# Optimization experiments

Hardware: AMD Instinct MI355X
Metric: run time of the kernel (lower is better)

The kernel has to match this reference:

```python
import math
import jax, jax.numpy as jnp
import numpy as np

H = 12          # num_attention_heads
D = 128         # head_dim = 1536 // 12
E = H * D       # hidden_size
CHUNK = 12      # attention_chunk_size
PAST = 12       # attention_context_left - 1
FUT = 0         # attention_context_right
CTX = CHUNK + PAST + FUT   # 24
CAP = 50.0      # attention_logit_cap
Q_SCALE = D ** (-0.5) / math.log(2.0)
K_SCALE = math.log(1.0 + math.e) / math.log(2.0)


def setup_inputs() -> dict:
    key = jax.random.key(0)
    ks = jax.random.split(key, 8)
    B, S = 8, 3072
    w_scale = E ** (-0.5)
    return {
        "hidden_states": jax.random.normal(ks[0], (B, S, E), jnp.float32),
        "position_embeddings": jax.random.normal(ks[1], (CTX, E), jnp.float32),
        "w_q": jax.random.normal(ks[2], (E, E), jnp.float32) * w_scale,
        "w_k": jax.random.normal(ks[3], (E, E), jnp.float32) * w_scale,
        "w_v": jax.random.normal(ks[4], (E, E), jnp.float32) * w_scale,
        "w_post": jax.random.normal(ks[5], (E, E), jnp.float32) * w_scale,
        "w_rel": jax.random.normal(ks[6], (E, E), jnp.float32) * w_scale,
        "per_dim_scale": jnp.zeros((D,), jnp.float32),
    }


def _rel_shift(x):
    # x: [B, H, nb, chunk, P] with P <= CTX+1 -> [B, H, nb, chunk, CTX]
    B, h, nb, bs, p = x.shape
    x = jnp.pad(x, ((0, 0), (0, 0), (0, 0), (0, 0), (0, CTX + 1 - p)))
    x = x.reshape(B, h, nb, bs * (CTX + 1))[..., : bs * CTX]
    return x.reshape(B, h, nb, bs, CTX)


def reference(hidden_states, position_embeddings, w_q, w_k, w_v, w_post, w_rel, per_dim_scale):
    B, S, _ = hidden_states.shape
    # projections (torch Linear: y = x @ W.T), computed in float32
    q = (hidden_states @ w_q.T).reshape(B, S, H, D)
    k = (hidden_states @ w_k.T).reshape(B, S, H, D)
    v = (hidden_states @ w_v.T).reshape(B, S, H, D)
    q = q * (Q_SCALE * jax.nn.softplus(per_dim_scale))  # per-dim query scale
    k = k * K_SCALE

    nb = (S + CHUNK - 1) // CHUNK
    pad = nb * CHUNK - S
    # convert_to_block: [B, nb, CHUNK, H, D]
    qb = jnp.pad(q, ((0, 0), (0, pad), (0, 0), (0, 0))).reshape(B, nb, CHUNK, H, D)

    def ctx_extract(x):
        # pad left by PAST, right by FUT + CHUNK - 1, then gather CTX-wide windows strided by CHUNK
        xp = jnp.pad(x, ((0, 0), (PAST, FUT + CHUNK - 1), (0, 0), (0, 0)))
        idx = jnp.arange(nb)[:, None] * CHUNK + jnp.arange(CTX)[None, :]
        return xp[:, idx]  # [B, nb, CTX, H, D]

    kc = ctx_extract(k)
    vc = ctx_extract(v)

    rel_k = (position_embeddings @ w_rel.T).reshape(-1, H, D)  # [P, H, D]

    # content term: [B, H, nb, CHUNK, CTX]
    ac = jnp.einsum('bnchd,bnkhd->bhnck', qb, kc)
    # position term + Transformer-XL rel shift
    bd = jnp.einsum('bnchd,phd->bhncp', qb, rel_k)
    bd = _rel_shift(bd)

    logits = ac + bd
    logits = jnp.tanh(logits / CAP) * CAP  # softcap
    attn_weights = jax.nn.softmax(logits, axis=-1)

    out = jnp.einsum('bhnck,bnkhd->bnchd', attn_weights, vc)
    out = out.reshape(B, nb * CHUNK, H * D)[:, :S]
    out = out @ w_post.T
    return out, attn_weights
```

## Files before the change

kernel.cpp:

```cpp
#include <hip/hip_runtime.h>
#include <hip/hip_bf16.h>

#define HH 12
#define DD 128
#define EE 1536
#define QKVP 4608
#define NBATCH 8
#define SEQ 3072
#define NBLK 256
#define CHK 12
#define CTXW 24
#define MTOK 24576

#define Q_SCALE_BASE 0.12751743f
#define K_SCALE_F 1.8946361322f

#define PITCH 65

typedef short s16x8 __attribute__((ext_vector_type(8)));
typedef float f32x4 __attribute__((ext_vector_type(4)));

__device__ __forceinline__ float bf2f(unsigned short u) {
  return __builtin_bit_cast(float, ((unsigned int)u) << 16);
}
__device__ __forceinline__ unsigned short f2bf(float f) {
  unsigned int u = __builtin_bit_cast(unsigned int, f);
  u += 0x7fffu + ((u >> 16) & 1u);
  return (unsigned short)(u >> 16);
}
__device__ __forceinline__ void bf2f2(unsigned int u, float& lo, float& hi) {
  lo = __builtin_bit_cast(float, u << 16);
  hi = __builtin_bit_cast(float, u & 0xffff0000u);
}

__device__ __forceinline__ void async16(const void* g, void* l) {
  __builtin_amdgcn_global_load_lds(
      (const __attribute__((address_space(1))) unsigned int*)g,
      (__attribute__((address_space(3))) unsigned int*)l, 16, 0, 0);
}

__global__ __launch_bounds__(256) void k_cvt(const float4* __restrict__ in,
                                             ushort4* __restrict__ out, int n4) {
  int i = blockIdx.x * 256 + threadIdx.x;
  if (i < n4) {
    float4 v = in[i];
    ushort4 o;
    o.x = f2bf(v.x); o.y = f2bf(v.y); o.z = f2bf(v.z); o.w = f2bf(v.w);
    out[i] = o;
  }
}

__global__ void k_qscale(const float* __restrict__ pds, float* __restrict__ qs) {
  int d = threadIdx.x;
  if (d < DD) {
    float x = pds[d];
    float sp = (x > 20.f) ? x : log1pf(expf(x));
    qs[d] = Q_SCALE_BASE * sp;
  }
}

__global__ __launch_bounds__(256) void k_rel(const float* __restrict__ pos,
                                             const float* __restrict__ w_rel,
                                             unsigned short* __restrict__ rel16) {
  __shared__ unsigned short lp[12 * EE];
  const int t = threadIdx.x;
  const int p0 = blockIdx.y * 12;
  for (int i = t; i < 12 * EE / 4; i += 256) {
    float4 x = ((const float4*)(pos + (long)p0 * EE))[i];
    ushort4 o; o.x = f2bf(x.x); o.y = f2bf(x.y); o.z = f2bf(x.z); o.w = f2bf(x.w);
    ((ushort4*)lp)[i] = o;
  }
  __syncthreads();
  const int col = blockIdx.x * 128 + (t & 127);
  const int pg = t >> 7;
  float acc[6] = {0.f, 0.f, 0.f, 0.f, 0.f, 0.f};
  const float* wr = w_rel + (long)col * EE;
  for (int e = 0; e < EE; ++e) {
    float w = wr[e];
#pragma unroll
    for (int i = 0; i < 6; ++i) acc[i] += w * bf2f(lp[(pg * 6 + i) * EE + e]);
  }
#pragma unroll
  for (int i = 0; i < 6; ++i)
    rel16[(long)(p0 + pg * 6 + i) * EE + col] = f2bf(acc[i]);
}


__device__ __forceinline__ void stage_half(const unsigned short* g0, long Kl,
                                           unsigned short* lhalf,
                                           int w, int rlo, int qz) {
  const unsigned short* s0 = g0 + (long)(w * 16 + rlo) * Kl + qz * 8;
  async16(s0,          lhalf + w * 1024);
  async16(s0 + 8 * Kl, lhalf + w * 1024 + 512);
}

__device__ __forceinline__ void tile4(
    unsigned short* AP, unsigned short* BP,
    unsigned short* AQ, unsigned short* BQ,
    const unsigned short* gAt, const unsigned short* gBt, long Kl,
    int t1, int t2, int w, int rlo, int qz,
    int aBase, int bBase, int sw0, int sw1, f32x4 (&acc)[8][4]) {
  s16x8 af[4], bf[4];

#pragma unroll
  for (int i = 0; i < 4; ++i) af[i] = *(const s16x8*)&AP[(aBase + 16 * i) * 64 + sw0];
#pragma unroll
  for (int j = 0; j < 4; ++j) bf[j] = *(const s16x8*)&BP[(bBase + 16 * j) * 64 + sw0];
  stage_half(gAt + (long)t1 * 64, Kl, AQ, w, rlo, qz);
  __builtin_amdgcn_s_barrier();
  __builtin_amdgcn_s_setprio(1);
#pragma unroll
  for (int i = 0; i < 4; ++i)
#pragma unroll
    for (int j = 0; j < 4; ++j)
      acc[i][j] = __builtin_amdgcn_mfma_f32_16x16x32_bf16(af[i], bf[j], acc[i][j], 0, 0, 0);
  __builtin_amdgcn_s_setprio(0);
  __builtin_amdgcn_s_barrier();

#pragma unroll
  for (int i = 0; i < 4; ++i) af[i] = *(const s16x8*)&AP[(aBase + 64 + 16 * i) * 64 + sw0];
  stage_half(gAt + 128 * Kl + (long)t1 * 64, Kl, AQ + 8192, w, rlo, qz);
  __builtin_amdgcn_s_barrier();
  __builtin_amdgcn_s_setprio(1);
#pragma unroll
  for (int i = 0; i < 4; ++i)
#pragma unroll
    for (int j = 0; j < 4; ++j)
      acc[4 + i][j] = __builtin_amdgcn_mfma_f32_16x16x32_bf16(af[i], bf[j], acc[4 + i][j], 0, 0, 0);
  __builtin_amdgcn_s_setprio(0);
  __builtin_amdgcn_s_barrier();

#pragma unroll
  for (int i = 0; i < 4; ++i) af[i] = *(const s16x8*)&AP[(aBase + 16 * i) * 64 + sw1];
#pragma unroll
  for (int j = 0; j < 4; ++j) bf[j] = *(const s16x8*)&BP[(bBase + 16 * j) * 64 + sw1];
  __builtin_amdgcn_s_barrier();
  __builtin_amdgcn_s_setprio(1);
#pragma unroll
  for (int i = 0; i < 4; ++i)
#pragma unroll
    for (int j = 0; j < 4; ++j)
      acc[i][j] = __builtin_amdgcn_mfma_f32_16x16x32_bf16(af[i], bf[j], acc[i][j], 0, 0, 0);
  __builtin_amdgcn_s_setprio(0);
  __builtin_amdgcn_s_barrier();

#pragma unroll
  for (int i = 0; i < 4; ++i) af[i] = *(const s16x8*)&AP[(aBase + 64 + 16 * i) * 64 + sw1];
  stage_half(gBt + (long)t2 * 64, Kl, BP, w, rlo, qz);
  stage_half(gBt + 128 * Kl + (long)t2 * 64, Kl, BP + 8192, w, rlo, qz);
  asm volatile("s_waitcnt vmcnt(4)" ::: "memory");
  __builtin_amdgcn_s_barrier();
  __builtin_amdgcn_s_setprio(1);
#pragma unroll
  for (int i = 0; i < 4; ++i)
#pragma unroll
    for (int j = 0; j < 4; ++j)
      acc[4 + i][j] = __builtin_amdgcn_mfma_f32_16x16x32_bf16(af[i], bf[j], acc[4 + i][j], 0, 0, 0);
  __builtin_amdgcn_s_setprio(0);
  __builtin_amdgcn_s_barrier();
}

__global__ __launch_bounds__(512, 2) void k_gemm256(
    const unsigned short* __restrict__ A, const unsigned short* __restrict__ Bt,
    void* __restrict__ Cv, int M, int N, int K, int gN,
    int mode, const float* __restrict__ qscale, int c_f32) {
  __shared__ unsigned short sm[65536];

  const int tid = threadIdx.x;
  const int w = tid >> 6;
  const int lane = tid & 63;
  const int quad = lane >> 4;
  const int l16 = lane & 15;
  const int sw = l16 & 7;
  const int rlo = lane >> 3;
  const int qz = (lane & 7) ^ rlo;

  const int nwg = gridDim.x;
  const int orig = blockIdx.x;
  const int qd = nwg >> 3;
  const int xcd = orig & 7;
  const int u = orig >> 3;
  const int bandsz = 4 * gN;
  const int band = u / bandsz;
  const int rem = u - band * bandsz;
  const int mi = band * 4 + (rem & 3);
  const int ni = rem >> 2;
  const int mloc = qd / gN;
  const int mt = xcd * mloc + mi;
  const int nt = ni;
  const long bm = (long)mt * 256, bn = (long)nt * 256;
  const long Kl = K;
  const unsigned short* gAt = A + bm * Kl;
  const unsigned short* gBt = Bt + bn * Kl;

  unsigned short* A0 = sm;
  unsigned short* B0 = sm + 16384;
  unsigned short* A1 = sm + 32768;
  unsigned short* B1 = sm + 49152;

  const int aBase = (w >> 2) * 128 + l16;
  const int bBase = (w & 3) * 64 + l16;
  const int sw0 = ((quad ^ sw) & 7) * 8;
  const int sw1 = (((4 | quad) ^ sw) & 7) * 8;

  f32x4 acc[8][4] = {};
  const int NT = K >> 6;

  stage_half(gAt,            Kl, A0,        w, rlo, qz);
  stage_half(gAt + 128 * Kl, Kl, A0 + 8192, w, rlo, qz);
  stage_half(gBt,            Kl, B0,        w, rlo, qz);
  stage_half(gBt + 128 * Kl, Kl, B0 + 8192, w, rlo, qz);
  stage_half(gBt + 64,            Kl, B1,        w, rlo, qz);
  stage_half(gBt + 128 * Kl + 64, Kl, B1 + 8192, w, rlo, qz);
  asm volatile("s_waitcnt vmcnt(4)" ::: "memory");
  __builtin_amdgcn_s_barrier();

  for (int t = 0; t < NT; t += 2) {
    const int t1 = t + 1;
    const int t2 = (t + 2 == NT) ? 0 : t + 2;
    const int t3 = (t + 3 >= NT) ? t + 3 - NT : t + 3;
    tile4(A0, B0, A1, B1, gAt, gBt, Kl, t1, t2, w, rlo, qz, aBase, bBase, sw0, sw1, acc);
    tile4(A1, B1, A0, B0, gAt, gBt, Kl, t2, t3, w, rlo, qz, aBase, bBase, sw0, sw1, acc);
  }

  __syncthreads();

  const int wmq = (w >> 2) * 128;
  const int wnq = (w & 3) * 64;

  if (!c_f32) {
#pragma unroll
    for (int j = 0; j < 4; ++j) {
      const long col = bn + wnq + 16 * j + l16;
      float scale = 1.0f;
      if (mode == 3)
        scale = (col < 1536) ? qscale[col & (DD - 1)] : (col < 3072 ? K_SCALE_F : 1.0f);
      const int lc = wnq + 16 * j + l16;
#pragma unroll
      for (int i = 0; i < 8; ++i) {
        const int lr0 = wmq + 16 * i + quad * 4;
#pragma unroll
        for (int r = 0; r < 4; ++r) {
          const int lr = lr0 + r;
          const int gsw = (lc >> 3) ^ ((lr >> 2) & 7);
          sm[lr * 256 + gsw * 8 + (lc & 7)] = f2bf(acc[i][j][r] * scale);
        }
      }
    }
    __syncthreads();
#pragma unroll
    for (int k = 0; k < 16; ++k) {
      const int G = k * 512 + tid;
      const int row = G >> 5, gc = G & 31;
      const int gsw = gc ^ ((row >> 2) & 7);
      s16x8 vdat = *(const s16x8*)&sm[row * 256 + gsw * 8];
      *(s16x8*)&((unsigned short*)Cv)[(bm + row) * (long)N + bn + gc * 8] = vdat;
    }
  } else {
    float* Cf = (float*)sm;
#pragma unroll
    for (int h = 0; h < 2; ++h) {
      if ((wmq == 0) == (h == 0)) {
#pragma unroll
        for (int j = 0; j < 4; ++j) {
          const long col = bn + wnq + 16 * j + l16;
          float scale = 1.0f;
          if (mode == 3)
            scale = (col < 1536) ? qscale[col & (DD - 1)] : (col < 3072 ? K_SCALE_F : 1.0f);
          const int lc = wnq + 16 * j + l16;
#pragma unroll
          for (int i = 0; i < 8; ++i) {
            const int lr0 = 16 * i + quad * 4;
#pragma unroll
            for (int r = 0; r < 4; ++r) {
              const int lr = lr0 + r;
              const int gsw = (lc >> 2) ^ ((lr >> 2) & 7);
              Cf[lr * 256 + gsw * 4 + (lc & 3)] = acc[i][j][r] * scale;
            }
          }
        }
      }
      __syncthreads();
#pragma unroll
      for (int k = 0; k < 16; ++k) {
        const int G = k * 512 + tid;
        const int row = G >> 6, gc = G & 63;
        const int gsw = gc ^ ((row >> 2) & 7);
        float4 vdat = *(const float4*)&Cf[row * 256 + gsw * 4];
        *(float4*)&((float*)Cv)[(bm + h * 128 + row) * (long)N + bn + gc * 4] = vdat;
      }
      __syncthreads();
    }
  }
}

__global__ __launch_bounds__(256) void k_attn(
    const unsigned short* __restrict__ qkv, const unsigned short* __restrict__ rel,
    unsigned short* __restrict__ attn_out, float* __restrict__ aw_out) {
  const int n = blockIdx.x;
  const int b = blockIdx.y;
  const int h = blockIdx.z;
  const int t = threadIdx.x;

  __shared__ unsigned int lq[CHK * PITCH];
  __shared__ unsigned int lk[CTXW * PITCH];
  __shared__ unsigned int lv[CTXW * PITCH];
  __shared__ unsigned int lr[CTXW * PITCH];
  __shared__ float sac[CHK * CTXW];
  __shared__ float sbd[CHK * CTXW];
  __shared__ float smax[CHK];
  __shared__ float sinv[CHK];

  const long tok0 = (long)b * SEQ + (long)n * CHK;
  const long hq = (long)h * DD;

  for (int u = t; u < CHK * 16; u += 256) {
    int r = u >> 4, w4 = u & 15;
    uint4 x = *(const uint4*)&qkv[(tok0 + r) * QKVP + hq + w4 * 8];
    unsigned int* d = &lq[r * PITCH + w4 * 4];
    d[0] = x.x; d[1] = x.y; d[2] = x.z; d[3] = x.w;
  }
  for (int u = t; u < CTXW * 16; u += 256) {
    int r = u >> 4, w4 = u & 15;
    int s = n * CHK + r - 12;
    uint4 kx, vx;
    if (s >= 0) {
      const unsigned short* base = &qkv[((long)b * SEQ + s) * QKVP + hq];
      kx = *(const uint4*)&base[1536 + w4 * 8];
      vx = *(const uint4*)&base[3072 + w4 * 8];
    } else {
      kx = make_uint4(0, 0, 0, 0);
      vx = make_uint4(0, 0, 0, 0);
    }
    uint4 rx = *(const uint4*)&rel[(long)r * EE + hq + w4 * 8];
    unsigned int* dk = &lk[r * PITCH + w4 * 4];
    unsigned int* dv = &lv[r * PITCH + w4 * 4];
    unsigned int* dr = &lr[r * PITCH + w4 * 4];
    dk[0] = kx.x; dk[1] = kx.y; dk[2] = kx.z; dk[3] = kx.w;
    dv[0] = vx.x; dv[1] = vx.y; dv[2] = vx.z; dv[3] = vx.w;
    dr[0] = rx.x; dr[1] = rx.y; dr[2] = rx.z; dr[3] = rx.w;
  }
  __syncthreads();

  for (int p = t; p < CHK * CTXW; p += 256) {
    int c = p / CTXW, j = p - c * CTXW;
    const unsigned int* uq = &lq[c * PITCH];
    const unsigned int* uk = &lk[j * PITCH];
    const unsigned int* ur = &lr[j * PITCH];
    float ac = 0.f, bd = 0.f;
#pragma unroll 16
    for (int d2 = 0; d2 < DD / 2; ++d2) {
      float a0, a1, k0f, k1f, r0, r1;
      bf2f2(uq[d2], a0, a1);
      bf2f2(uk[d2], k0f, k1f);
      bf2f2(ur[d2], r0, r1);
      ac += a0 * k0f + a1 * k1f;
      bd += a0 * r0 + a1 * r1;
    }
    sac[p] = ac;
    sbd[p] = bd;
  }
  __syncthreads();

  for (int p = t; p < CHK * CTXW; p += 256) {
    int c = p / CTXW, j = p - c * CTXW;
    float y;
    if (j >= c) y = sbd[c * CTXW + (j - c)];
    else if (j == c - 1) y = 0.f;
    else y = sbd[(c - 1) * CTXW + (j - c + CTXW + 1)];
    float x = (sac[p] + y) * 0.02f;
    x = fminf(fmaxf(x, -15.f), 15.f);
    float e2 = __expf(2.f * x);
    sac[p] = 50.f * (e2 - 1.f) / (e2 + 1.f);
  }
  __syncthreads();

  if (t < CHK) {
    float m = -3.0e38f;
#pragma unroll
    for (int j = 0; j < CTXW; ++j) m = fmaxf(m, sac[t * CTXW + j]);
    smax[t] = m;
  }
  __syncthreads();

  for (int p = t; p < CHK * CTXW; p += 256) {
    int c = p / CTXW;
    sbd[p] = __expf(sac[p] - smax[c]);
  }
  __syncthreads();

  if (t < CHK) {
    float s = 0.f;
#pragma unroll
    for (int j = 0; j < CTXW; ++j) s += sbd[t * CTXW + j];
    sinv[t] = 1.f / s;
  }
  __syncthreads();

  for (int p = t; p < CHK * CTXW; p += 256) {
    int c = p / CTXW, j = p - c * CTXW;
    float w = sbd[p] * sinv[c];
    sac[p] = w;
    aw_out[((((long)b * HH + h) * NBLK + n) * CHK + c) * CTXW + j] = w;
  }
  __syncthreads();

  for (int p = t; p < CHK * (DD / 2); p += 256) {
    int c = p >> 6, d2 = p & 63;
    float a0 = 0.f, a1 = 0.f;
#pragma unroll
    for (int j = 0; j < CTXW; ++j) {
      float w = sac[c * CTXW + j];
      float v0, v1;
      bf2f2(lv[j * PITCH + d2], v0, v1);
      a0 += w * v0; a1 += w * v1;
    }
    unsigned int packed = ((unsigned int)f2bf(a1) << 16) | (unsigned int)f2bf(a0);
    *(unsigned int*)&attn_out[(tok0 + c) * EE + hq + d2 * 2] = packed;
  }
}

extern "C" void kernel_launch(void* const* d_in, const int* in_sizes, int n_in,
                              void* d_out, int out_size, void* d_ws, size_t ws_size,
                              hipStream_t stream) {
  const float* hs     = (const float*)d_in[0];
  const float* pos    = (const float*)d_in[1];
  const float* w_q    = (const float*)d_in[2];
  const float* w_k    = (const float*)d_in[3];
  const float* w_v    = (const float*)d_in[4];
  const float* w_post = (const float*)d_in[5];
  const float* w_rel  = (const float*)d_in[6];
  const float* pds    = (const float*)d_in[7];

  char* ws = (char*)d_ws;
  const size_t TOKB = (size_t)MTOK * EE * 2;
  const size_t WB   = (size_t)EE * EE * 2;
  unsigned short* hs16   = (unsigned short*)(ws);
  unsigned short* qkv16  = (unsigned short*)(ws + TOKB);
  unsigned short* wq16   = (unsigned short*)(ws + 4 * TOKB);
  unsigned short* wk16   = (unsigned short*)(ws + 4 * TOKB + WB);
  unsigned short* wv16   = (unsigned short*)(ws + 4 * TOKB + 2 * WB);
  unsigned short* wp16   = (unsigned short*)(ws + 4 * TOKB + 3 * WB);
  unsigned short* rel16  = (unsigned short*)(ws + 4 * TOKB + 4 * WB);
  float* qscale          = (float*)(ws + 4 * TOKB + 4 * WB + CTXW * EE * 2);
  unsigned short* attn16 = hs16;

  float* out = (float*)d_out;
  float* aw  = out + (size_t)MTOK * EE;

  k_cvt<<<36864, 256, 0, stream>>>((const float4*)hs, (ushort4*)hs16, MTOK * EE / 4);
  k_cvt<<<2304, 256, 0, stream>>>((const float4*)w_q, (ushort4*)wq16, EE * EE / 4);
  k_cvt<<<2304, 256, 0, stream>>>((const float4*)w_k, (ushort4*)wk16, EE * EE / 4);
  k_cvt<<<2304, 256, 0, stream>>>((const float4*)w_v, (ushort4*)wv16, EE * EE / 4);
  k_cvt<<<2304, 256, 0, stream>>>((const float4*)w_post, (ushort4*)wp16, EE * EE / 4);
  k_qscale<<<1, 128, 0, stream>>>(pds, qscale);
  k_rel<<<dim3(12, 2), 256, 0, stream>>>(pos, w_rel, rel16);

  k_gemm256<<<dim3((MTOK / 256) * (QKVP / 256)), 512, 0, stream>>>(
      hs16, wq16, qkv16, MTOK, QKVP, EE, QKVP / 256, 3, qscale, 0);

  k_attn<<<dim3(NBLK, NBATCH, HH), 256, 0, stream>>>(qkv16, rel16, attn16, aw);

  k_gemm256<<<dim3((MTOK / 256) * (EE / 256)), 512, 0, stream>>>(
      attn16, wp16, out, MTOK, EE, EE, EE / 256, 0, nullptr, 1);
}
```

Before: 1.033 ms.

## Use MFMA for attention QK/PV and vectorize relative-position projection

Rewrites the chunked attention kernel so the content and position logits (Q·K and Q·rel) and the weights-times-V product run as bf16 16x16x32 MFMA instructions, replacing scalar per-thread dot products. Q, K and rel tiles are stored in XOR-swizzled LDS, and V is stored transposed so it can serve as an MFMA operand. The k_rel kernel also reads w_rel as float4 and LDS as packed pairs to cut per-element load overhead. The softmax weights are now rounded to bf16 before the PV product, which slightly lowers precision, and the padded tile rows are left uninitialized, though they only feed results that are discarded.

```diff
diff --git a/kernel.cpp b/kernel.cpp
--- a/kernel.cpp
+++ b/kernel.cpp
@@ -15,8 +15,6 @@
 #define Q_SCALE_BASE 0.12751743f
 #define K_SCALE_F 1.8946361322f
 
-#define PITCH 65
-
 typedef short s16x8 __attribute__((ext_vector_type(8)));
 typedef float f32x4 __attribute__((ext_vector_type(4)));
 
@@ -75,10 +73,17 @@
   const int pg = t >> 7;
   float acc[6] = {0.f, 0.f, 0.f, 0.f, 0.f, 0.f};
   const float* wr = w_rel + (long)col * EE;
-  for (int e = 0; e < EE; ++e) {
-    float w = wr[e];
-#pragma unroll
-    for (int i = 0; i < 6; ++i) acc[i] += w * bf2f(lp[(pg * 6 + i) * EE + e]);
+  for (int e = 0; e < EE; e += 4) {
+    float4 w4 = *(const float4*)&wr[e];
+#pragma unroll
+    for (int i = 0; i < 6; ++i) {
+      const unsigned short* lpr = &lp[(pg * 6 + i) * EE + e];
+      unsigned int u01 = *(const unsigned int*)lpr;
+      unsigned int u23 = *(const unsigned int*)(lpr + 2);
+      float a0, a1, a2, a3;
+      bf2f2(u01, a0, a1); bf2f2(u23, a2, a3);
+      acc[i] += w4.x * a0 + w4.y * a1 + w4.z * a2 + w4.w * a3;
+    }
   }
 #pragma unroll
   for (int i = 0; i < 6; ++i)
@@ -301,122 +306,139 @@
   const int b = blockIdx.y;
   const int h = blockIdx.z;
   const int t = threadIdx.x;
-
-  __shared__ unsigned int lq[CHK * PITCH];
-  __shared__ unsigned int lk[CTXW * PITCH];
-  __shared__ unsigned int lv[CTXW * PITCH];
-  __shared__ unsigned int lr[CTXW * PITCH];
-  __shared__ float sac[CHK * CTXW];
-  __shared__ float sbd[CHK * CTXW];
-  __shared__ float smax[CHK];
-  __shared__ float sinv[CHK];
+  const int wv = t >> 6;
+  const int lane = t & 63;
+  const int quad = lane >> 4;
+  const int l16 = lane & 15;
+
+  __shared__ unsigned short lq[16 * 128];
+  __shared__ unsigned short lk[32 * 128];
+  __shared__ unsigned short lrel[32 * 128];
+  __shared__ unsigned short lvt[128 * 40];
+  __shared__ unsigned short lw[16 * 40];
+  __shared__ float sac[16 * 33];
+  __shared__ float sbd[16 * 33];
+  __shared__ unsigned short sO[12 * 136];
+  __shared__ float smax[12], sinv[12];
 
   const long tok0 = (long)b * SEQ + (long)n * CHK;
   const long hq = (long)h * DD;
 
-  for (int u = t; u < CHK * 16; u += 256) {
+  for (int u = t; u < 192; u += 256) {
     int r = u >> 4, w4 = u & 15;
     uint4 x = *(const uint4*)&qkv[(tok0 + r) * QKVP + hq + w4 * 8];
-    unsigned int* d = &lq[r * PITCH + w4 * 4];
-    d[0] = x.x; d[1] = x.y; d[2] = x.z; d[3] = x.w;
-  }
-  for (int u = t; u < CTXW * 16; u += 256) {
+    *(uint4*)&lq[r * 128 + ((w4 ^ (r & 7)) * 8)] = x;
+  }
+  for (int u = t; u < 384; u += 256) {
     int r = u >> 4, w4 = u & 15;
     int s = n * CHK + r - 12;
-    uint4 kx, vx;
-    if (s >= 0) {
-      const unsigned short* base = &qkv[((long)b * SEQ + s) * QKVP + hq];
-      kx = *(const uint4*)&base[1536 + w4 * 8];
-      vx = *(const uint4*)&base[3072 + w4 * 8];
-    } else {
-      kx = make_uint4(0, 0, 0, 0);
-      vx = make_uint4(0, 0, 0, 0);
-    }
+    uint4 kx = make_uint4(0, 0, 0, 0);
+    if (s >= 0) kx = *(const uint4*)&qkv[((long)b * SEQ + s) * QKVP + hq + 1536 + w4 * 8];
+    *(uint4*)&lk[r * 128 + ((w4 ^ (r & 7)) * 8)] = kx;
     uint4 rx = *(const uint4*)&rel[(long)r * EE + hq + w4 * 8];
-    unsigned int* dk = &lk[r * PITCH + w4 * 4];
-    unsigned int* dv = &lv[r * PITCH + w4 * 4];
-    unsigned int* dr = &lr[r * PITCH + w4 * 4];
-    dk[0] = kx.x; dk[1] = kx.y; dk[2] = kx.z; dk[3] = kx.w;
-    dv[0] = vx.x; dv[1] = vx.y; dv[2] = vx.z; dv[3] = vx.w;
-    dr[0] = rx.x; dr[1] = rx.y; dr[2] = rx.z; dr[3] = rx.w;
-  }
-  __syncthreads();
-
-  for (int p = t; p < CHK * CTXW; p += 256) {
-    int c = p / CTXW, j = p - c * CTXW;
-    const unsigned int* uq = &lq[c * PITCH];
-    const unsigned int* uk = &lk[j * PITCH];
-    const unsigned int* ur = &lr[j * PITCH];
-    float ac = 0.f, bd = 0.f;
-#pragma unroll 16
-    for (int d2 = 0; d2 < DD / 2; ++d2) {
-      float a0, a1, k0f, k1f, r0, r1;
-      bf2f2(uq[d2], a0, a1);
-      bf2f2(uk[d2], k0f, k1f);
-      bf2f2(ur[d2], r0, r1);
-      ac += a0 * k0f + a1 * k1f;
-      bd += a0 * r0 + a1 * r1;
-    }
-    sac[p] = ac;
-    sbd[p] = bd;
+    *(uint4*)&lrel[r * 128 + ((w4 ^ (r & 7)) * 8)] = rx;
+  }
+  for (int u = t; u < 384; u += 256) {
+    int r = u >> 4, d16 = u & 15, d0 = d16 * 8;
+    int s = n * CHK + r - 12;
+    uint4 vx = make_uint4(0, 0, 0, 0);
+    if (s >= 0) vx = *(const uint4*)&qkv[((long)b * SEQ + s) * QKVP + hq + 3072 + d0];
+    unsigned short vs[8];
+    *(uint4*)vs = vx;
+#pragma unroll
+    for (int i = 0; i < 8; ++i) {
+      int ii = (i + d16) & 7;
+      lvt[(d0 + ii) * 40 + r] = vs[ii];
+    }
+  }
+  for (int u = t; u < 128; u += 256)
+    *(uint4*)&lvt[u * 40 + 24] = make_uint4(0, 0, 0, 0);
+  for (int u = t; u < 80; u += 256)
+    *(uint4*)&lw[u * 8] = make_uint4(0, 0, 0, 0);
+  __syncthreads();
+
+  {
+    const unsigned short* bsrc = (wv < 2) ? lk : lrel;
+    const int nt = wv & 1;
+    f32x4 acc = {};
+#pragma unroll
+    for (int dc = 0; dc < 4; ++dc) {
+      const int g = dc * 4 + quad;
+      s16x8 a = *(const s16x8*)&lq[l16 * 128 + ((g ^ (l16 & 7)) * 8)];
+      const int rB = nt * 16 + l16;
+      s16x8 bb = *(const s16x8*)&bsrc[rB * 128 + ((g ^ (rB & 7)) * 8)];
+      acc = __builtin_amdgcn_mfma_f32_16x16x32_bf16(a, bb, acc, 0, 0, 0);
+    }
+    float* dstp = (wv < 2) ? sac : sbd;
+#pragma unroll
+    for (int r = 0; r < 4; ++r)
+      dstp[(quad * 4 + r) * 33 + nt * 16 + l16] = acc[r];
   }
   __syncthreads();
 
   for (int p = t; p < CHK * CTXW; p += 256) {
     int c = p / CTXW, j = p - c * CTXW;
     float y;
-    if (j >= c) y = sbd[c * CTXW + (j - c)];
+    if (j >= c) y = sbd[c * 33 + (j - c)];
     else if (j == c - 1) y = 0.f;
-    else y = sbd[(c - 1) * CTXW + (j - c + CTXW + 1)];
-    float x = (sac[p] + y) * 0.02f;
+    else y = sbd[(c - 1) * 33 + (j - c + CTXW + 1)];
+    float x = (sac[c * 33 + j] + y) * 0.02f;
     x = fminf(fmaxf(x, -15.f), 15.f);
     float e2 = __expf(2.f * x);
-    sac[p] = 50.f * (e2 - 1.f) / (e2 + 1.f);
+    sac[c * 33 + j] = 50.f * (e2 - 1.f) / (e2 + 1.f);
   }
   __syncthreads();
 
   if (t < CHK) {
     float m = -3.0e38f;
 #pragma unroll
-    for (int j = 0; j < CTXW; ++j) m = fmaxf(m, sac[t * CTXW + j]);
+    for (int j = 0; j < CTXW; ++j) m = fmaxf(m, sac[t * 33 + j]);
     smax[t] = m;
   }
   __syncthreads();
 
   for (int p = t; p < CHK * CTXW; p += 256) {
-    int c = p / CTXW;
-    sbd[p] = __expf(sac[p] - smax[c]);
+    int c = p / CTXW, j = p - c * CTXW;
+    sbd[c * 33 + j] = __expf(sac[c * 33 + j] - smax[c]);
   }
   __syncthreads();
 
   if (t < CHK) {
     float s = 0.f;
 #pragma unroll
-    for (int j = 0; j < CTXW; ++j) s += sbd[t * CTXW + j];
+    for (int j = 0; j < CTXW; ++j) s += sbd[t * 33 + j];
     sinv[t] = 1.f / s;
   }
   __syncthreads();
 
   for (int p = t; p < CHK * CTXW; p += 256) {
     int c = p / CTXW, j = p - c * CTXW;
-    float w = sbd[p] * sinv[c];
-    sac[p] = w;
-    aw_out[((((long)b * HH + h) * NBLK + n) * CHK + c) * CTXW + j] = w;
-  }
-  __syncthreads();
-
-  for (int p = t; p < CHK * (DD / 2); p += 256) {
-    int c = p >> 6, d2 = p & 63;
-    float a0 = 0.f, a1 = 0.f;
-#pragma unroll
-    for (int j = 0; j < CTXW; ++j) {
-      float w = sac[c * CTXW + j];
-      float v0, v1;
-      bf2f2(lv[j * PITCH + d2], v0, v1);
-      a0 += w * v0; a1 += w * v1;
-    }
-    unsigned int packed = ((unsigned int)f2bf(a1) << 16) | (unsigned int)f2bf(a0);
-    *(unsigned int*)&attn_out[(tok0 + c) * EE + hq + d2 * 2] = packed;
+    float wgt = sbd[c * 33 + j] * sinv[c];
+    aw_out[((((long)b * HH + h) * NBLK + n) * CHK + c) * CTXW + j] = wgt;
+    lw[c * 40 + j] = f2bf(wgt);
+  }
+  __syncthreads();
+
+  {
+    s16x8 afw = *(const s16x8*)&lw[l16 * 40 + quad * 8];
+#pragma unroll
+    for (int e = 0; e < 2; ++e) {
+      const int dnt = wv * 2 + e;
+      s16x8 bv = *(const s16x8*)&lvt[(dnt * 16 + l16) * 40 + quad * 8];
+      f32x4 o = __builtin_amdgcn_mfma_f32_16x16x32_bf16(afw, bv, (f32x4){}, 0, 0, 0);
+#pragma unroll
+      for (int r = 0; r < 4; ++r) {
+        const int row = quad * 4 + r;
+        if (row < CHK) sO[row * 136 + dnt * 16 + l16] = f2bf(o[r]);
+      }
+    }
+  }
+  __syncthreads();
+
+  for (int u = t; u < 192; u += 256) {
+    int r = u >> 4, w4 = u & 15;
+    uint4 x = *(const uint4*)&sO[r * 136 + w4 * 8];
+    *(uint4*)&attn_out[(tok0 + r) * EE + hq + w4 * 8] = x;
   }
 }
 
```

New measurement: 987.3 us. -4.4%, faster.
